# Optimization experiments

Hardware: AMD Instinct MI355X
Metric: run time of the kernel (lower is better)

## Reference

```python
import jax, jax.numpy as jnp
import numpy as np

CAPACITY = 0.125


def setup_inputs() -> dict:
    key = jax.random.key(0)
    ks = jax.random.split(key, 6)
    b, s, d, dff = 4, 8192, 512, 2048
    x = jax.random.normal(ks[0], (b, s, d), dtype=jnp.float32)
    position_ids = jnp.tile(jnp.arange(s, dtype=jnp.int64)[None, :], (b, 1))
    Wr = jax.random.normal(ks[1], (d,), dtype=jnp.float32) * 0.02
    br = jnp.zeros((1,), dtype=jnp.float32)
    W1 = jax.random.normal(ks[2], (d, dff), dtype=jnp.float32) * 0.02
    b1 = jnp.zeros((dff,), dtype=jnp.float32)
    W2 = jax.random.normal(ks[3], (dff, d), dtype=jnp.float32) * 0.02
    b2 = jnp.zeros((d,), dtype=jnp.float32)
    return {"x": x, "position_ids": position_ids, "Wr": Wr, "br": br,
            "W1": W1, "b1": b1, "W2": W2, "b2": b2}


def reference(x, position_ids, Wr, br, W1, b1, W2, b2):
    b, s, d = x.shape
    # Router: Linear(d, 1) -> squeeze(-1)
    weights = jnp.einsum('bsd,d->bs', x, Wr) + br  # [b, s]
    k = int(CAPACITY * s)
    # Per-batch top-k threshold (k-th largest value)
    top_k_values = jax.lax.top_k(weights, k)[0]  # [b, k], sorted desc
    threshold = top_k_values[:, -1]              # [b]
    selected_mask = weights > threshold[:, None]  # strict >, ties excluded (matches torch)
    # Block: per-token MLP (Linear-GELU-Linear). Per-token ops commute with the
    # gather/scatter, so computing densely and masking is mathematically identical
    # to the original gather -> block -> weighted scatter.
    h = jax.nn.gelu(jnp.einsum('bsd,df->bsf', x, W1) + b1)
    y = jnp.einsum('bsf,fd->bsd', h, W2) + b2
    # processed_tokens (= block_out * router_weight on selected) + x on unselected
    out = jnp.where(selected_mask[..., None], y * weights[..., None], x)
    return out
```

## Files before the change

### kernel.cpp

```cpp
#include <hip/hip_runtime.h>
#include <hip/hip_bf16.h>

#define B_   4
#define S_   8192
#define D_   512
#define DFF_ 2048
#define K_TOP 1024

typedef unsigned short u16;
typedef __attribute__((ext_vector_type(8))) short bf16x8;
typedef __attribute__((ext_vector_type(4))) float floatx4;

__device__ __forceinline__ unsigned f2key(float f){
    unsigned u = __float_as_uint(f);
    return (u & 0x80000000u) ? ~u : (u | 0x80000000u);
}
__device__ __forceinline__ u16 f2b(float f){
    unsigned u = __float_as_uint(f);
    u = (u + 0x7FFFu + ((u >> 16) & 1u)) >> 16;
    return (u16)u;
}
__device__ __forceinline__ float gelu_fast(float v){
    float u = 1.5957691216f * v + 0.0713548162726f * v * v * v;
    float e = __expf(u);
    return v - v / (e + 1.0f);
}
__device__ __forceinline__ void gl_lds16(const void* gptr, void* lptr){
    auto g = (const __attribute__((address_space(1))) unsigned int*)((uintptr_t)gptr);
    auto l = (__attribute__((address_space(3))) unsigned int*)((uintptr_t)lptr);
    __builtin_amdgcn_global_load_lds(g, l, 16, 0, 0);
}


__global__ __launch_bounds__(256) void prep_kernel(
    const float* __restrict__ W1, const float* __restrict__ W2,
    u16* __restrict__ W1t, u16* __restrict__ W2t,
    const float4* __restrict__ x, float4* __restrict__ out,
    const float4* __restrict__ Wr4, const float* __restrict__ br,
    float* __restrict__ w_all, unsigned* __restrict__ ghist)
{
    __shared__ __align__(16) unsigned char shmem[128 * 132 * 2];
    const int tid = threadIdx.x;
    const int bx = blockIdx.x;
    if (bx < 128){
        const float* src; u16* dst; int R, C, ct, ks;
        if (bx < 64){ src = W1; dst = W1t; R = D_;   C = DFF_; ct = bx & 15;        ks = bx >> 4; }
        else        { src = W2; dst = W2t; R = DFF_; C = D_;   ct = (bx - 64) & 3;  ks = (bx - 64) >> 2; }
        u16 (*tile)[132] = (u16(*)[132])shmem;
        #pragma unroll
        for (int it = 0; it < 64; it++){
            int lin = it * 256 + tid;
            int kk = lin >> 7, nn = lin & 127;
            tile[kk][nn] = f2b(src[(size_t)(ks * 128 + kk) * C + ct * 128 + nn]);
        }
        __syncthreads();
        u16* base = dst + (size_t)(ct * (R / 128) + ks) * 16384;
        const int r = tid >> 1, h = tid & 1;
        #pragma unroll
        for (int c = 0; c < 8; c++){
            int cl = h * 8 + c;
            bf16x8 bv;
            #pragma unroll
            for (int e = 0; e < 8; e++) bv[e] = (short)tile[cl * 8 + e][r];
            *(bf16x8*)&base[r * 128 + ((cl ^ (r & 15)) << 3)] = bv;
        }
    } else {
        unsigned* hist = (unsigned*)shmem;
        if (tid < 256) hist[tid] = 0u;
        __syncthreads();
        const int wb = bx - 128;
        const int wv = tid >> 6, lane = tid & 63;
        const int t0 = wb * 64 + wv * 16;
        const float brv = br[0];
        #pragma unroll 2
        for (int tk = 0; tk < 16; tk++){
            int token = t0 + tk;
            const float4* xt = x + (size_t)token * 128;
            float4* ot = out + (size_t)token * 128;
            float acc = 0.f;
            #pragma unroll
            for (int i = 0; i < 2; i++){
                int j = lane + i * 64;
                float4 v = xt[j];
                ot[j] = v;
                float4 wv4 = Wr4[j];
                acc += v.x*wv4.x + v.y*wv4.y + v.z*wv4.z + v.w*wv4.w;
            }
            #pragma unroll
            for (int off = 32; off > 0; off >>= 1) acc += __shfl_down(acc, off, 64);
            if (lane == 0){
                float wt = acc + brv;
                w_all[token] = wt;
                atomicAdd(&hist[f2key(wt) >> 24], 1u);
            }
        }
        __syncthreads();
        if (tid < 256) ghist[wb * 256 + tid] = hist[tid];
    }
}

__global__ __launch_bounds__(1024) void kth_compact_kernel(
    const float4* __restrict__ w_all4, const unsigned* __restrict__ ghist,
    int* __restrict__ counts, int* __restrict__ idx)
{
    __shared__ unsigned keys[S_];
    __shared__ unsigned hist[16][256];
    __shared__ unsigned suffix[256];
    __shared__ unsigned sprefix;
    __shared__ int sremk;
    __shared__ int lbase;
    const int b = blockIdx.x, tid = threadIdx.x, wv = tid >> 6;
    const float4* row4 = w_all4 + (size_t)b * (S_ / 4);

    #pragma unroll
    for (int i = 0; i < 2; i++){
        int j = tid + i * 1024;
        float4 v = row4[j];
        keys[4*j+0] = f2key(v.x); keys[4*j+1] = f2key(v.y);
        keys[4*j+2] = f2key(v.z); keys[4*j+3] = f2key(v.w);
    }
    if (tid < 256){
        unsigned s = 0;
        const unsigned* gh = ghist + (size_t)(b * 128) * 256 + tid;
        #pragma unroll 8
        for (int j = 0; j < 128; j++) s += gh[j * 256];
        suffix[tid] = s;
    }
    if (tid == 0) lbase = 0;
    __syncthreads();
    for (int off = 1; off < 256; off <<= 1){
        unsigned v = 0;
        if (tid < 256 && tid + off < 256) v = suffix[tid + off];
        __syncthreads();
        if (tid < 256) suffix[tid] += v;
        __syncthreads();
    }
    if (tid < 256){
        unsigned snext = (tid == 255) ? 0u : suffix[tid + 1];
        if (suffix[tid] >= (unsigned)K_TOP && snext < (unsigned)K_TOP){
            sprefix = ((unsigned)tid) << 24;
            sremk = K_TOP - (int)snext;
        }
    }
    __syncthreads();

    for (int pass = 2; pass >= 0; pass--){
        for (int i = tid; i < 16 * 256; i += 1024) ((unsigned*)hist)[i] = 0u;
        __syncthreads();
        const unsigned mask_hi = 0xFFFFFFFFu << ((pass + 1) * 8);
        const unsigned pfx = sprefix;
        const int shift = pass * 8;
        #pragma unroll
        for (int i = 0; i < 8; i++){
            unsigned key = keys[tid + i * 1024];
            if ((key & mask_hi) == pfx)
                atomicAdd(&hist[wv][(key >> shift) & 255u], 1u);
        }
        __syncthreads();
        if (tid < 256){
            unsigned s = 0;
            #pragma unroll
            for (int h = 0; h < 16; h++) s += hist[h][tid];
            suffix[tid] = s;
        }
        __syncthreads();
        for (int off = 1; off < 256; off <<= 1){
            unsigned v = 0;
            if (tid < 256 && tid + off < 256) v = suffix[tid + off];
            __syncthreads();
            if (tid < 256) suffix[tid] += v;
            __syncthreads();
        }
        const int remk = sremk;
        __syncthreads();
        if (tid < 256){
            unsigned snext = (tid == 255) ? 0u : suffix[tid + 1];
            if (suffix[tid] >= (unsigned)remk && snext < (unsigned)remk){
                sprefix = pfx | ((unsigned)tid << shift);
                sremk = remk - (int)snext;
            }
        }
        __syncthreads();
    }

    const unsigned thr = sprefix;
    #pragma unroll
    for (int i = 0; i < 8; i++){
        int li = tid + i * 1024;
        bool sel = keys[li] > thr;
        unsigned long long m = __ballot(sel);
        int wtot = (int)__popcll(m);
        if (wtot){
            int woff = 0;
            if ((tid & 63) == 0) woff = atomicAdd(&lbase, wtot);
            woff = __shfl(woff, 0, 64);
            if (sel){
                int pos = woff + (int)__popcll(m & ((1ull << (tid & 63)) - 1ull));
                idx[b * 1024 + pos] = b * S_ + li;
            }
        }
    }
    __syncthreads();
    if (tid == 0) counts[b] = lbase;
}

__global__ __launch_bounds__(256) void gather_kernel(
    const float* __restrict__ x, const int* __restrict__ idx,
    const int* __restrict__ counts, u16* __restrict__ XbT)
{
    const int mt = blockIdx.x, s = blockIdx.y;
    const int cl = threadIdx.x & 15, r16 = threadIdx.x >> 4;
    u16* base = XbT + (size_t)(mt * 4 + s) * 16384;
    #pragma unroll
    for (int it = 0; it < 8; it++){
        int r = r16 + it * 16;
        int mg = mt * 128 + r;
        if ((mg & 1023) < counts[mg >> 10]){
            const float* xp = x + (size_t)idx[mg] * D_ + s * 128 + cl * 8;
            float4 v0 = *(const float4*)xp;
            float4 v1 = *(const float4*)(xp + 4);
            bf16x8 bv;
            bv[0]=(short)f2b(v0.x); bv[1]=(short)f2b(v0.y);
            bv[2]=(short)f2b(v0.z); bv[3]=(short)f2b(v0.w);
            bv[4]=(short)f2b(v1.x); bv[5]=(short)f2b(v1.y);
            bv[6]=(short)f2b(v1.z); bv[7]=(short)f2b(v1.w);
            *(bf16x8*)&base[r * 128 + ((cl ^ (r & 15)) << 3)] = bv;
        }
    }
}

__global__ __launch_bounds__(256) void ffn1_kernel(
    const u16* __restrict__ XbT, const u16* __restrict__ W1t,
    const int* __restrict__ counts, const float* __restrict__ bias1,
    u16* __restrict__ Ht)
{
    __shared__ __align__(16) u16 smem[32768];
    const int tid = threadIdx.x;
    const int mBlk = blockIdx.x, nBlk = blockIdx.y;
    const int lane = tid & 63, w = tid >> 6;
    const int wr = (w >> 1) * 64, wc = (w & 1) * 64;
    const int fr = lane & 15, quad = lane >> 4;

    const char* Abase = (const char*)(XbT + (size_t)mBlk * 4 * 16384);
    const char* Bbase = (const char*)(W1t + (size_t)nBlk * 4 * 16384);
    char* Al0 = (char*)smem + tid * 16;
    char* Bl0 = (char*)(smem + 16384) + tid * 16;
    const int rr0 = tid >> 3, pp = tid & 7;

    auto stage = [&](const char* gbase, char* lb, int hs){
        const char* s0 = gbase + (size_t)(hs >> 1) * 32768;
        const int h = hs & 1;
        #pragma unroll
        for (int i = 0; i < 4; i++){
            int r = rr0 + i * 32;
            int pg = pp | (((h ^ (r >> 3)) & 1) << 3);
            gl_lds16(s0 + r * 256 + pg * 16, lb + i * 4096);
        }
    };

    stage(Abase, Al0, 0);
    stage(Bbase, Bl0, 0);

    floatx4 acc[4][4] = {};
    for (int hs = 0; hs < 8; hs++){
        __syncthreads();
        if (hs + 1 < 8){
            stage(Abase, Al0 + ((hs + 1) & 1) * 16384, hs + 1);
            stage(Bbase, Bl0 + ((hs + 1) & 1) * 16384, hs + 1);
        }
        const u16* Ab = smem + (hs & 1) * 8192;
        const u16* Bb = smem + 16384 + (hs & 1) * 8192;
        #pragma unroll
        for (int ks2 = 0; ks2 < 2; ks2++){
            bf16x8 af[4], bf[4];
            #pragma unroll
            for (int i = 0; i < 4; i++){
                int r = wr + i * 16 + fr;
                af[i] = *(const bf16x8*)&Ab[r * 64 + (((ks2 * 4 + quad) ^ (r & 7)) << 3)];
            }
            #pragma unroll
            for (int j = 0; j < 4; j++){
                int r = wc + j * 16 + fr;
                bf[j] = *(const bf16x8*)&Bb[r * 64 + (((ks2 * 4 + quad) ^ (r & 7)) << 3)];
            }
            #pragma unroll
            for (int i = 0; i < 4; i++)
                #pragma unroll
                for (int j = 0; j < 4; j++)
                    acc[i][j] = __builtin_amdgcn_mfma_f32_16x16x32_bf16(af[i], bf[j], acc[i][j], 0, 0, 0);
        }
    }

    float bj[4];
    #pragma unroll
    for (int j = 0; j < 4; j++) bj[j] = bias1[nBlk * 128 + wc + j * 16 + fr];

    __syncthreads();
    u16* Cs = smem;
    #pragma unroll
    for (int i = 0; i < 4; i++){
        #pragma unroll
        for (int rg = 0; rg < 4; rg++){
            int r = wr + i * 16 + quad * 4 + rg;
            #pragma unroll
            for (int j = 0; j < 4; j++){
                int col = wc + j * 16 + fr;
                float v = gelu_fast(acc[i][j][rg] + bj[j]);
                Cs[r * 128 + ((((col >> 3) ^ (r & 15)) << 3) | (col & 7))] = f2b(v);
            }
        }
    }
    __syncthreads();
    const int r = tid >> 1, h = tid & 1;
    int mg = mBlk * 128 + r;
    if ((mg & 1023) < counts[mg >> 10]){
        u16* dstp = Ht + (((size_t)(mBlk * 2 + (r >> 6)) * 16 + nBlk) * 64 + (r & 63)) * 128;
        #pragma unroll
        for (int p = 0; p < 8; p++){
            int pc = h * 8 + p;
            *(bf16x8*)&dstp[pc << 3] = *(const bf16x8*)&Cs[r * 128 + (pc << 3)];
        }
    }
}

__global__ __launch_bounds__(256) void ffn2_kernel(
    const u16* __restrict__ Ht, const u16* __restrict__ W2t,
    const int* __restrict__ counts, const int* __restrict__ idx,
    const float* __restrict__ w_all, const float* __restrict__ bias2,
    float* __restrict__ out)
{
    __shared__ __align__(16) u16 smem[24576];
    const int tid = threadIdx.x;
    const int mBlk = blockIdx.x, nBlk = blockIdx.y;
    const int lane = tid & 63, w = tid >> 6;
    const int wr = (w >> 1) * 32, wc = (w & 1) * 64;
    const int fr = lane & 15, quad = lane >> 4;

    const char* Abase = (const char*)(Ht + (size_t)mBlk * 16 * 8192);
    const char* Bbase = (const char*)(W2t + (size_t)nBlk * 16 * 16384);
    char* Al0 = (char*)smem + tid * 16;
    char* Bl0 = (char*)(smem + 8192) + tid * 16;
    const int rr0 = tid >> 3, pp = tid & 7;

    auto stageA = [&](int buf, int hs){
        const char* s0 = Abase + (size_t)(hs >> 1) * 16384;
        const int h = hs & 1;
        char* l = Al0 + buf * 8192;
        #pragma unroll
        for (int i = 0; i < 2; i++){
            int r = rr0 + i * 32;
            int pg = pp | (((h ^ (r >> 3)) & 1) << 3);
            gl_lds16(s0 + r * 256 + pg * 16, l + i * 4096);
        }
    };
    auto stageB = [&](int buf, int hs){
        const char* s0 = Bbase + (size_t)(hs >> 1) * 32768;
        const int h = hs & 1;
        char* l = Bl0 + buf * 16384;
        #pragma unroll
        for (int i = 0; i < 4; i++){
            int r = rr0 + i * 32;
            int pg = pp | (((h ^ (r >> 3)) & 1) << 3);
            gl_lds16(s0 + r * 256 + pg * 16, l + i * 4096);
        }
    };

    stageA(0, 0); stageB(0, 0);
    floatx4 acc[2][4] = {};
    for (int hs = 0; hs < 32; hs++){
        __syncthreads();
        if (hs + 1 < 32){ stageA((hs + 1) & 1, hs + 1); stageB((hs + 1) & 1, hs + 1); }
        const u16* Ab = smem + (hs & 1) * 4096;
        const u16* Bb = smem + 8192 + (hs & 1) * 8192;
        #pragma unroll
        for (int ks2 = 0; ks2 < 2; ks2++){
            bf16x8 af[2], bf[4];
            #pragma unroll
            for (int i = 0; i < 2; i++){
                int r = wr + i * 16 + fr;
                af[i] = *(const bf16x8*)&Ab[r * 64 + (((ks2 * 4 + quad) ^ (r & 7)) << 3)];
            }
            #pragma unroll
            for (int j = 0; j < 4; j++){
                int r = wc + j * 16 + fr;
                bf[j] = *(const bf16x8*)&Bb[r * 64 + (((ks2 * 4 + quad) ^ (r & 7)) << 3)];
            }
            #pragma unroll
            for (int i = 0; i < 2; i++)
                #pragma unroll
                for (int j = 0; j < 4; j++)
                    acc[i][j] = __builtin_amdgcn_mfma_f32_16x16x32_bf16(af[i], bf[j], acc[i][j], 0, 0, 0);
        }
    }

    float bj[4];
    #pragma unroll
    for (int j = 0; j < 4; j++) bj[j] = bias2[nBlk * 128 + wc + j * 16 + fr];

    __syncthreads();
    float* Cs = (float*)smem;
    #pragma unroll
    for (int i = 0; i < 2; i++){
        #pragma unroll
        for (int rg = 0; rg < 4; rg++){
            int r = wr + i * 16 + quad * 4 + rg;
            #pragma unroll
            for (int j = 0; j < 4; j++)
                Cs[r * 128 + wc + j * 16 + fr] = acc[i][j][rg] + bj[j];
        }
    }
    __syncthreads();
    const int r = tid >> 2, q = tid & 3;
    int mg = mBlk * 64 + r;
    if ((mg & 1023) < counts[mg >> 10]){
        int token = idx[mg];
        float wt = w_all[token];
        float* op = out + (size_t)token * D_ + nBlk * 128 + q * 32;
        const float4* cp = (const float4*)&Cs[r * 128 + q * 32];
        #pragma unroll
        for (int p = 0; p < 8; p++){
            float4 vv = cp[p];
            vv.x *= wt; vv.y *= wt; vv.z *= wt; vv.w *= wt;
            ((float4*)op)[p] = vv;
        }
    }
}

extern "C" void kernel_launch(void* const* d_in, const int* in_sizes, int n_in,
                              void* d_out, int out_size, void* d_ws, size_t ws_size,
                              hipStream_t stream)
{
    const float* x  = (const float*)d_in[0];
    const float* Wr = (const float*)d_in[2];
    const float* br = (const float*)d_in[3];
    const float* W1 = (const float*)d_in[4];
    const float* b1 = (const float*)d_in[5];
    const float* W2 = (const float*)d_in[6];
    const float* b2 = (const float*)d_in[7];
    float* out = (float*)d_out;
    char* ws = (char*)d_ws;

    float*    w_all  = (float*)   (ws + 0);
    int*      counts = (int*)     (ws + 131072);
    int*      idx    = (int*)     (ws + 131136);
    unsigned* ghist  = (unsigned*)(ws + 163840);
    u16*      XbT    = (u16*)     (ws + 720896);
    u16*      W1t    = (u16*)     (ws + 4915200);
    u16*      W2t    = (u16*)     (ws + 7012352);
    u16*      Ht     = (u16*)     (ws + 9109504);

    prep_kernel<<<640, 256, 0, stream>>>(
        W1, W2, W1t, W2t, (const float4*)x, (float4*)out,
        (const float4*)Wr, br, w_all, ghist);
    kth_compact_kernel<<<B_, 1024, 0, stream>>>(
        (const float4*)w_all, ghist, counts, idx);
    gather_kernel<<<dim3(32, 4), 256, 0, stream>>>(x, idx, counts, XbT);
    ffn1_kernel<<<dim3(32, DFF_/128), 256, 0, stream>>>(XbT, W1t, counts, b1, Ht);
    ffn2_kernel<<<dim3(64, D_/128),   256, 0, stream>>>(Ht, W2t, counts, idx, w_all, b2, out);
}
```

Before: 193.6 us.

## Move unselected-token copy into FFN grids and streamline radix select

The copy of x to out leaves the router prep kernel. Only unselected tokens are now copied, by extra blocks appended to the ffn1 and ffn2 grids, which overlaps the copy with the GEMMs and stops the write for selected tokens. The kth-select kernel now does its prefix scans with wave shuffles, uses fewer histogram copies and stores the threshold. The GEMM loops swap __syncthreads for explicit vmcnt waits, split barriers and setprio. The router dot product is also batched four tokens at a time.

```diff
diff --git a/kernel.cpp b/kernel.cpp
--- a/kernel.cpp
+++ b/kernel.cpp
@@ -35,7 +35,7 @@
 __global__ __launch_bounds__(256) void prep_kernel(
     const float* __restrict__ W1, const float* __restrict__ W2,
     u16* __restrict__ W1t, u16* __restrict__ W2t,
-    const float4* __restrict__ x, float4* __restrict__ out,
+    const float4* __restrict__ x,
     const float4* __restrict__ Wr4, const float* __restrict__ br,
     float* __restrict__ w_all, unsigned* __restrict__ ghist)
 {
@@ -72,26 +72,29 @@
         const int wv = tid >> 6, lane = tid & 63;
         const int t0 = wb * 64 + wv * 16;
         const float brv = br[0];
-        #pragma unroll 2
-        for (int tk = 0; tk < 16; tk++){
-            int token = t0 + tk;
-            const float4* xt = x + (size_t)token * 128;
-            float4* ot = out + (size_t)token * 128;
-            float acc = 0.f;
-            #pragma unroll
-            for (int i = 0; i < 2; i++){
-                int j = lane + i * 64;
-                float4 v = xt[j];
-                ot[j] = v;
-                float4 wv4 = Wr4[j];
-                acc += v.x*wv4.x + v.y*wv4.y + v.z*wv4.z + v.w*wv4.w;
-            }
-            #pragma unroll
-            for (int off = 32; off > 0; off >>= 1) acc += __shfl_down(acc, off, 64);
+        const float4 wr0 = Wr4[lane], wr1 = Wr4[lane + 64];
+        #pragma unroll
+        for (int g = 0; g < 4; g++){
+            float a[4];
+            #pragma unroll
+            for (int tt = 0; tt < 4; tt++){
+                const float4* xt = x + (size_t)(t0 + g * 4 + tt) * 128;
+                float4 v0 = xt[lane], v1 = xt[lane + 64];
+                a[tt] = v0.x*wr0.x + v0.y*wr0.y + v0.z*wr0.z + v0.w*wr0.w
+                      + v1.x*wr1.x + v1.y*wr1.y + v1.z*wr1.z + v1.w*wr1.w;
+            }
+            #pragma unroll
+            for (int off = 32; off > 0; off >>= 1){
+                #pragma unroll
+                for (int tt = 0; tt < 4; tt++) a[tt] += __shfl_down(a[tt], off, 64);
+            }
             if (lane == 0){
-                float wt = acc + brv;
-                w_all[token] = wt;
-                atomicAdd(&hist[f2key(wt) >> 24], 1u);
+                #pragma unroll
+                for (int tt = 0; tt < 4; tt++){
+                    float wt = a[tt] + brv;
+                    w_all[t0 + g * 4 + tt] = wt;
+                    atomicAdd(&hist[f2key(wt) >> 24], 1u);
+                }
             }
         }
         __syncthreads();
@@ -101,15 +104,16 @@
 
 __global__ __launch_bounds__(1024) void kth_compact_kernel(
     const float4* __restrict__ w_all4, const unsigned* __restrict__ ghist,
-    int* __restrict__ counts, int* __restrict__ idx)
+    int* __restrict__ counts, unsigned* __restrict__ thr_out,
+    int* __restrict__ idx)
 {
     __shared__ unsigned keys[S_];
-    __shared__ unsigned hist[16][256];
-    __shared__ unsigned suffix[256];
+    __shared__ unsigned hist[4][256];
     __shared__ unsigned sprefix;
     __shared__ int sremk;
     __shared__ int lbase;
-    const int b = blockIdx.x, tid = threadIdx.x, wv = tid >> 6;
+    const int b = blockIdx.x, tid = threadIdx.x;
+    const int wv = tid >> 6, lane = tid & 63;
     const float4* row4 = w_all4 + (size_t)b * (S_ / 4);
 
     #pragma unroll
@@ -119,65 +123,58 @@
         keys[4*j+0] = f2key(v.x); keys[4*j+1] = f2key(v.y);
         keys[4*j+2] = f2key(v.z); keys[4*j+3] = f2key(v.w);
     }
-    if (tid < 256){
+    {
+        const int bin = tid & 255, q = tid >> 8;
         unsigned s = 0;
-        const unsigned* gh = ghist + (size_t)(b * 128) * 256 + tid;
+        const unsigned* gh = ghist + (size_t)(b * 128 + q * 32) * 256 + bin;
         #pragma unroll 8
-        for (int j = 0; j < 128; j++) s += gh[j * 256];
-        suffix[tid] = s;
-    }
-    if (tid == 0) lbase = 0;
+        for (int j = 0; j < 32; j++) s += gh[j * 256];
+        hist[q][bin] = s;
+    }
+    if (tid == 0){ sprefix = 0u; sremk = K_TOP; lbase = 0; }
     __syncthreads();
-    for (int off = 1; off < 256; off <<= 1){
-        unsigned v = 0;
-        if (tid < 256 && tid + off < 256) v = suffix[tid + off];
-        __syncthreads();
-        if (tid < 256) suffix[tid] += v;
-        __syncthreads();
-    }
-    if (tid < 256){
-        unsigned snext = (tid == 255) ? 0u : suffix[tid + 1];
-        if (suffix[tid] >= (unsigned)K_TOP && snext < (unsigned)K_TOP){
-            sprefix = ((unsigned)tid) << 24;
-            sremk = K_TOP - (int)snext;
-        }
-    }
-    __syncthreads();
-
-    for (int pass = 2; pass >= 0; pass--){
-        for (int i = tid; i < 16 * 256; i += 1024) ((unsigned*)hist)[i] = 0u;
-        __syncthreads();
-        const unsigned mask_hi = 0xFFFFFFFFu << ((pass + 1) * 8);
-        const unsigned pfx = sprefix;
+
+    for (int pass = 3; pass >= 0; pass--){
         const int shift = pass * 8;
-        #pragma unroll
-        for (int i = 0; i < 8; i++){
-            unsigned key = keys[tid + i * 1024];
-            if ((key & mask_hi) == pfx)
-                atomicAdd(&hist[wv][(key >> shift) & 255u], 1u);
-        }
-        __syncthreads();
-        if (tid < 256){
-            unsigned s = 0;
-            #pragma unroll
-            for (int h = 0; h < 16; h++) s += hist[h][tid];
-            suffix[tid] = s;
-        }
-        __syncthreads();
-        for (int off = 1; off < 256; off <<= 1){
-            unsigned v = 0;
-            if (tid < 256 && tid + off < 256) v = suffix[tid + off];
+        if (pass < 3){
+            ((unsigned*)hist)[tid] = 0u;
             __syncthreads();
-            if (tid < 256) suffix[tid] += v;
+            const unsigned mask_hi = 0xFFFFFFFFu << (shift + 8);
+            const unsigned pfx = sprefix;
+            #pragma unroll
+            for (int i = 0; i < 8; i++){
+                unsigned key = keys[tid + i * 1024];
+                if ((key & mask_hi) == pfx)
+                    atomicAdd(&hist[wv & 3][(key >> shift) & 255u], 1u);
+            }
             __syncthreads();
         }
-        const int remk = sremk;
-        __syncthreads();
-        if (tid < 256){
-            unsigned snext = (tid == 255) ? 0u : suffix[tid + 1];
-            if (suffix[tid] >= (unsigned)remk && snext < (unsigned)remk){
-                sprefix = pfx | ((unsigned)tid << shift);
-                sremk = remk - (int)snext;
+        if (wv == 0){
+            const unsigned remk = (unsigned)sremk;
+            const unsigned pfx = sprefix;
+            unsigned c[4];
+            #pragma unroll
+            for (int q = 0; q < 4; q++)
+                c[q] = hist[0][4*lane+q] + hist[1][4*lane+q]
+                     + hist[2][4*lane+q] + hist[3][4*lane+q];
+            unsigned t = c[0] + c[1] + c[2] + c[3];
+            unsigned ss = t;
+            #pragma unroll
+            for (int off = 1; off < 64; off <<= 1){
+                unsigned o = __shfl_down(ss, off, 64);
+                ss += (lane + off < 64) ? o : 0u;
+            }
+            const unsigned sgt = ss - t;
+            unsigned suf[4];
+            suf[3] = c[3] + sgt; suf[2] = c[2] + suf[3];
+            suf[1] = c[1] + suf[2]; suf[0] = c[0] + suf[1];
+            #pragma unroll
+            for (int q = 0; q < 4; q++){
+                unsigned nx = suf[q] - c[q];
+                if (suf[q] >= remk && nx < remk){
+                    sprefix = pfx | ((unsigned)(4 * lane + q) << shift);
+                    sremk = (int)(remk - nx);
+                }
             }
         }
         __syncthreads();
@@ -192,16 +189,16 @@
         int wtot = (int)__popcll(m);
         if (wtot){
             int woff = 0;
-            if ((tid & 63) == 0) woff = atomicAdd(&lbase, wtot);
+            if (lane == 0) woff = atomicAdd(&lbase, wtot);
             woff = __shfl(woff, 0, 64);
             if (sel){
-                int pos = woff + (int)__popcll(m & ((1ull << (tid & 63)) - 1ull));
+                int pos = woff + (int)__popcll(m & ((1ull << lane) - 1ull));
                 idx[b * 1024 + pos] = b * S_ + li;
             }
         }
     }
     __syncthreads();
-    if (tid == 0) counts[b] = lbase;
+    if (tid == 0){ counts[b] = lbase; thr_out[b] = thr; }
 }
 
 __global__ __launch_bounds__(256) void gather_kernel(
@@ -229,14 +226,41 @@
     }
 }
 
+__device__ __forceinline__ void copy_unselected(
+    const float4* __restrict__ x, float4* __restrict__ out,
+    const float* __restrict__ w_all, const unsigned* __restrict__ thr,
+    int cIdx, int tid)
+{
+    const int wv = tid >> 6, lane = tid & 63;
+    const int tBase = cIdx * 128 + wv * 32;
+    #pragma unroll 2
+    for (int tt = 0; tt < 32; tt++){
+        int t = tBase + tt;
+        float wt = w_all[t];
+        if (f2key(wt) <= thr[t >> 13]){
+            const float4* xs = x + (size_t)t * 128;
+            float4* od = out + (size_t)t * 128;
+            od[lane]      = xs[lane];
+            od[lane + 64] = xs[lane + 64];
+        }
+    }
+}
+
 __global__ __launch_bounds__(256) void ffn1_kernel(
     const u16* __restrict__ XbT, const u16* __restrict__ W1t,
     const int* __restrict__ counts, const float* __restrict__ bias1,
-    u16* __restrict__ Ht)
+    u16* __restrict__ Ht,
+    const float4* __restrict__ x, float4* __restrict__ out,
+    const float* __restrict__ w_all, const unsigned* __restrict__ thr)
 {
     __shared__ __align__(16) u16 smem[32768];
     const int tid = threadIdx.x;
-    const int mBlk = blockIdx.x, nBlk = blockIdx.y;
+    const int bx = blockIdx.x;
+    if (bx >= 512){
+        copy_unselected(x, out, w_all, thr, bx - 512, tid);
+        return;
+    }
+    const int mBlk = bx & 31, nBlk = bx >> 5;
     const int lane = tid & 63, w = tid >> 6;
     const int wr = (w >> 1) * 64, wc = (w & 1) * 64;
     const int fr = lane & 15, quad = lane >> 4;
@@ -263,13 +287,19 @@
 
     floatx4 acc[4][4] = {};
     for (int hs = 0; hs < 8; hs++){
-        __syncthreads();
+        __builtin_amdgcn_s_barrier();
         if (hs + 1 < 8){
             stage(Abase, Al0 + ((hs + 1) & 1) * 16384, hs + 1);
             stage(Bbase, Bl0 + ((hs + 1) & 1) * 16384, hs + 1);
-        }
+            asm volatile("s_waitcnt vmcnt(8)" ::: "memory");
+        } else {
+            asm volatile("s_waitcnt vmcnt(0)" ::: "memory");
+        }
+        __builtin_amdgcn_sched_barrier(0);
+        __builtin_amdgcn_s_barrier();
         const u16* Ab = smem + (hs & 1) * 8192;
         const u16* Bb = smem + 16384 + (hs & 1) * 8192;
+        __builtin_amdgcn_s_setprio(1);
         #pragma unroll
         for (int ks2 = 0; ks2 < 2; ks2++){
             bf16x8 af[4], bf[4];
@@ -289,6 +319,7 @@
                 for (int j = 0; j < 4; j++)
                     acc[i][j] = __builtin_amdgcn_mfma_f32_16x16x32_bf16(af[i], bf[j], acc[i][j], 0, 0, 0);
         }
+        __builtin_amdgcn_s_setprio(0);
     }
 
     float bj[4];
@@ -327,11 +358,17 @@
     const u16* __restrict__ Ht, const u16* __restrict__ W2t,
     const int* __restrict__ counts, const int* __restrict__ idx,
     const float* __restrict__ w_all, const float* __restrict__ bias2,
-    float* __restrict__ out)
+    float* __restrict__ out,
+    const float4* __restrict__ x, const unsigned* __restrict__ thr)
 {
     __shared__ __align__(16) u16 smem[24576];
     const int tid = threadIdx.x;
-    const int mBlk = blockIdx.x, nBlk = blockIdx.y;
+    const int bx = blockIdx.x;
+    if (bx >= 256){
+        copy_unselected(x, (float4*)out, w_all, thr, 128 + (bx - 256), tid);
+        return;
+    }
+    const int mBlk = bx & 63, nBlk = bx >> 6;
     const int lane = tid & 63, w = tid >> 6;
     const int wr = (w >> 1) * 32, wc = (w & 1) * 64;
     const int fr = lane & 15, quad = lane >> 4;
@@ -342,36 +379,45 @@
     char* Bl0 = (char*)(smem + 8192) + tid * 16;
     const int rr0 = tid >> 3, pp = tid & 7;
 
-    auto stageA = [&](int buf, int hs){
-        const char* s0 = Abase + (size_t)(hs >> 1) * 16384;
+    auto stage = [&](int buf, int hs){
         const int h = hs & 1;
-        char* l = Al0 + buf * 8192;
-        #pragma unroll
-        for (int i = 0; i < 2; i++){
-            int r = rr0 + i * 32;
-            int pg = pp | (((h ^ (r >> 3)) & 1) << 3);
-            gl_lds16(s0 + r * 256 + pg * 16, l + i * 4096);
+        {
+            const char* s0 = Abase + (size_t)(hs >> 1) * 16384;
+            char* l = Al0 + buf * 8192;
+            #pragma unroll
+            for (int i = 0; i < 2; i++){
+                int r = rr0 + i * 32;
+                int pg = pp | (((h ^ (r >> 3)) & 1) << 3);
+                gl_lds16(s0 + r * 256 + pg * 16, l + i * 4096);
+            }
+        }
+        {
+            const char* s0 = Bbase + (size_t)(hs >> 1) * 32768;
+            char* l = Bl0 + buf * 16384;
+            #pragma unroll
+            for (int i = 0; i < 4; i++){
+                int r = rr0 + i * 32;
+                int pg = pp | (((h ^ (r >> 3)) & 1) << 3);
+                gl_lds16(s0 + r * 256 + pg * 16, l + i * 4096);
+            }
         }
     };
-    auto stageB = [&](int buf, int hs){
-        const char* s0 = Bbase + (size_t)(hs >> 1) * 32768;
-        const int h = hs & 1;
-        char* l = Bl0 + buf * 16384;
-        #pragma unroll
-        for (int i = 0; i < 4; i++){
-            int r = rr0 + i * 32;
-            int pg = pp | (((h ^ (r >> 3)) & 1) << 3);
-            gl_lds16(s0 + r * 256 + pg * 16, l + i * 4096);
-        }
-    };
-
-    stageA(0, 0); stageB(0, 0);
+
+    stage(0, 0);
     floatx4 acc[2][4] = {};
     for (int hs = 0; hs < 32; hs++){
-        __syncthreads();
-        if (hs + 1 < 32){ stageA((hs + 1) & 1, hs + 1); stageB((hs + 1) & 1, hs + 1); }
+        __builtin_amdgcn_s_barrier();
+        if (hs + 1 < 32){
+            stage((hs + 1) & 1, hs + 1);
+            asm volatile("s_waitcnt vmcnt(6)" ::: "memory");
+        } else {
+            asm volatile("s_waitcnt vmcnt(0)" ::: "memory");
+        }
+        __builtin_amdgcn_sched_barrier(0);
+        __builtin_amdgcn_s_barrier();
         const u16* Ab = smem + (hs & 1) * 4096;
         const u16* Bb = smem + 8192 + (hs & 1) * 8192;
+        __builtin_amdgcn_s_setprio(1);
         #pragma unroll
         for (int ks2 = 0; ks2 < 2; ks2++){
             bf16x8 af[2], bf[4];
@@ -391,6 +437,7 @@
                 for (int j = 0; j < 4; j++)
                     acc[i][j] = __builtin_amdgcn_mfma_f32_16x16x32_bf16(af[i], bf[j], acc[i][j], 0, 0, 0);
         }
+        __builtin_amdgcn_s_setprio(0);
     }
 
     float bj[4];
@@ -442,6 +489,7 @@
 
     float*    w_all  = (float*)   (ws + 0);
     int*      counts = (int*)     (ws + 131072);
+    unsigned* thr    = (unsigned*)(ws + 131088);
     int*      idx    = (int*)     (ws + 131136);
     unsigned* ghist  = (unsigned*)(ws + 163840);
     u16*      XbT    = (u16*)     (ws + 720896);
@@ -450,11 +498,13 @@
     u16*      Ht     = (u16*)     (ws + 9109504);
 
     prep_kernel<<<640, 256, 0, stream>>>(
-        W1, W2, W1t, W2t, (const float4*)x, (float4*)out,
+        W1, W2, W1t, W2t, (const float4*)x,
         (const float4*)Wr, br, w_all, ghist);
     kth_compact_kernel<<<B_, 1024, 0, stream>>>(
-        (const float4*)w_all, ghist, counts, idx);
+        (const float4*)w_all, ghist, counts, thr, idx);
     gather_kernel<<<dim3(32, 4), 256, 0, stream>>>(x, idx, counts, XbT);
-    ffn1_kernel<<<dim3(32, DFF_/128), 256, 0, stream>>>(XbT, W1t, counts, b1, Ht);
-    ffn2_kernel<<<dim3(64, D_/128),   256, 0, stream>>>(Ht, W2t, counts, idx, w_all, b2, out);
-}
+    ffn1_kernel<<<640, 256, 0, stream>>>(
+        XbT, W1t, counts, b1, Ht, (const float4*)x, (float4*)out, w_all, thr);
+    ffn2_kernel<<<384, 256, 0, stream>>>(
+        Ht, W2t, counts, idx, w_all, b2, out, (const float4*)x, thr);
+}
```

Result: no change. 197.0 us (+1.7%).
